# Performance work log

Hardware: AMD Instinct MI355X
Metric: run time of the kernel (lower is better)

## Reference

```python
import jax, jax.numpy as jnp
import numpy as np

# --- module constants (from init_kwargs) ---
R_HRS = 1000000.0   # high-resistance state (ohm)
R_LRS = 1000.0      # low-resistance state (ohm)
PARASITIC_R = 2.0   # wire resistance per crossbar segment (ohm)
BITS = 4            # conductance quantization bits
BATCH, IN_F, OUT_F = 8192, 1024, 1024


def weight_mapping(W, R_hrs, R_lrs):
    # linearly map weights into the [G_hrs, G_lrs] conductance window
    G_hrs, G_lrs = 1.0 / R_hrs, 1.0 / R_lrs
    Wmin, Wmax = W.min(), W.max()
    return (W - Wmin) / (Wmax - Wmin) * (G_lrs - G_hrs) + G_hrs


def quantization(G, R_lrs, R_hrs, bits):
    # snap conductances to 2**bits uniform levels in [G_hrs, G_lrs]
    G_hrs, G_lrs = 1.0 / R_hrs, 1.0 / R_lrs
    step = (G_lrs - G_hrs) / (2 ** bits - 1)
    return jnp.round((G - G_hrs) / step) * step + G_hrs


def ideal_model(G, x, parasitic_r):
    # ideal crossbar: I = V @ G  (no IR drop)
    return x @ G


def jeong_model(G, x, parasitic_r):
    # Jeong-style analytical IR-drop model: each cell (i, j) sees an extra
    # series wire resistance r*((j+1) segments along its word line +
    # (rows - i) segments along its bit line).
    rows, cols = G.shape  # [in, out]
    r_series = parasitic_r * (
        (jnp.arange(cols, dtype=G.dtype) + 1.0)[None, :]
        + (rows - jnp.arange(rows, dtype=G.dtype))[:, None]
    )  # [in, out]
    G_eff = 1.0 / (1.0 / G + r_series)
    return x @ G_eff  # [batch, out]


def output_unmapping(Wt, currents, x, R_hrs, R_lrs):
    # invert the affine conductance mapping: G = a*W + b  =>  x@W = (I - b*sum(x))/a
    G_hrs, G_lrs = 1.0 / R_hrs, 1.0 / R_lrs
    Wmin, Wmax = Wt.min(), Wt.max()
    a = (G_lrs - G_hrs) / (Wmax - Wmin)
    b = G_hrs - a * Wmin
    return (currents - b * x.sum(axis=1, keepdims=True)) / a


def setup_inputs() -> dict:
    key = jax.random.key(0)
    k1, k2, k3 = jax.random.split(key, 3)
    x = jax.random.uniform(k1, (BATCH, IN_F), dtype=jnp.float32)          # read voltages in [0,1)
    weight = jax.random.normal(k2, (OUT_F, IN_F), dtype=jnp.float32) * 0.1
    bias = jax.random.normal(k3, (OUT_F,), dtype=jnp.float32) * 0.01
    return {"x": x, "weight": weight, "bias": bias}


def reference(x, weight, bias):
    Wt = weight.T  # [in, out], matches self.weight.T in the torch module
    conductances = quantization(weight_mapping(Wt, R_HRS, R_LRS), R_LRS, R_HRS, BITS)
    currents = jeong_model(conductances, x, PARASITIC_R)          # non-ideal simulation
    ideal_currents = ideal_model(conductances, x, PARASITIC_R)    # bias-correction pass
    correction = currents.mean(axis=1) / ideal_currents.mean(axis=1)  # [batch]
    output = output_unmapping(Wt, currents, x, R_HRS, R_LRS)      # [batch, out]
    return output + bias[None, :] * correction[:, None]
```

## Files before the change

### kernel.cpp

```cpp
#include <hip/hip_runtime.h>
#include <hip/hip_bf16.h>
#include <cstdint>

#define BATCH 8192
#define IN_F  1024
#define OUT_F 1024
#define G_HRS 1e-6f
#define G_LRS 1e-3f
#define PAR_R 2.0f
#define LEVELS 15.0f

#define WS_PMIN  0
#define WS_PMAX  1024
#define WS_VEFF  4096
#define WS_VID   8192
#define WS_CORR  16384
#define WS_BT    65536
#define WS_ABF   (65536 + 2097152)
#define WS_NEED_FULL  ((size_t)WS_ABF + (size_t)BATCH * IN_F * 2)

__device__ __forceinline__ unsigned short f2bf(float f) {
    union { float f; unsigned int i; } v; v.f = f;
    unsigned int u = v.i;
    unsigned int r = (u + 0x7FFFu + ((u >> 16) & 1u)) >> 16;
    return (unsigned short)r;
}
__device__ __forceinline__ float quant_g(float wv, float wmin, float inv_range) {
    float t = (wv - wmin) * inv_range;
    float step = (G_LRS - G_HRS) / LEVELS;
    return rintf(t * LEVELS) * step + G_HRS;
}

__global__ void kprep(const float* __restrict__ w, float* __restrict__ pmin, float* __restrict__ pmax,
                      float* __restrict__ veff, float* __restrict__ vid) {
    int tid = blockIdx.x * blockDim.x + threadIdx.x;
    float lo = 1e30f, hi = -1e30f;
    const float4* w4 = (const float4*)w;
    const int n4 = (IN_F * OUT_F) / 4;
    for (int i = tid; i < n4; i += 256 * 256) {
        float4 q = w4[i];
        lo = fminf(lo, fminf(fminf(q.x, q.y), fminf(q.z, q.w)));
        hi = fmaxf(hi, fmaxf(fmaxf(q.x, q.y), fmaxf(q.z, q.w)));
    }
#pragma unroll
    for (int m = 1; m < 64; m <<= 1) {
        lo = fminf(lo, __shfl_xor(lo, m, 64));
        hi = fmaxf(hi, __shfl_xor(hi, m, 64));
    }
    __shared__ float slo[4], shi[4];
    int wv = threadIdx.x >> 6, ln = threadIdx.x & 63;
    if (ln == 0) { slo[wv] = lo; shi[wv] = hi; }
    __syncthreads();
    if (threadIdx.x == 0) {
        pmin[blockIdx.x] = fminf(fminf(slo[0], slo[1]), fminf(slo[2], slo[3]));
        pmax[blockIdx.x] = fmaxf(fmaxf(shi[0], shi[1]), fmaxf(shi[2], shi[3]));
    }
    if (blockIdx.x == 0) {
        float4 z = make_float4(0.f, 0.f, 0.f, 0.f);
        ((float4*)veff)[threadIdx.x] = z;
        ((float4*)vid)[threadIdx.x]  = z;
    }
}

__global__ void kbuildvec(const float* __restrict__ w, const float* __restrict__ pmin,
                          const float* __restrict__ pmax, unsigned short* __restrict__ bt,
                          float* __restrict__ veff, float* __restrict__ vid) {
    float lo = pmin[threadIdx.x], hi = pmax[threadIdx.x];
#pragma unroll
    for (int m = 1; m < 64; m <<= 1) {
        lo = fminf(lo, __shfl_xor(lo, m, 64));
        hi = fmaxf(hi, __shfl_xor(hi, m, 64));
    }
    __shared__ float slo[4], shi[4];
    int wv = threadIdx.x >> 6, ln = threadIdx.x & 63;
    if (ln == 0) { slo[wv] = lo; shi[wv] = hi; }
    __syncthreads();
    float wmin = fminf(fminf(slo[0], slo[1]), fminf(slo[2], slo[3]));
    float wmax = fmaxf(fmaxf(shi[0], shi[1]), fmaxf(shi[2], shi[3]));

    float inv_range = 1.0f / (wmax - wmin);
    float acoef = (G_LRS - G_HRS) * inv_range;
    float bcoef = G_HRS - acoef * wmin;
    float inva = 1.0f / acoef;

    int k0 = threadIdx.x * 4;
    float se[4] = {0.f, 0.f, 0.f, 0.f}, si[4] = {0.f, 0.f, 0.f, 0.f};
#pragma unroll
    for (int rr = 0; rr < 16; rr++) {
        int n = blockIdx.x * 16 + rr;
        float4 q = *(const float4*)&w[(size_t)n * IN_F + k0];
        float wvv[4] = { q.x, q.y, q.z, q.w };
        unsigned short o[4];
#pragma unroll
        for (int j = 0; j < 4; j++) {
            int k = k0 + j;
            float g = quant_g(wvv[j], wmin, inv_range);
            float r = PAR_R * ((float)(n + 1) + (float)(IN_F - k));
            float ge = 1.0f / (1.0f / g + r);
            o[j] = f2bf((ge - bcoef) * inva);
            se[j] += ge;
            si[j] += g;
        }
        uint2 ov;
        ov.x = (unsigned int)o[0] | ((unsigned int)o[1] << 16);
        ov.y = (unsigned int)o[2] | ((unsigned int)o[3] << 16);
        *(uint2*)&bt[(size_t)n * IN_F + k0] = ov;
    }
#pragma unroll
    for (int j = 0; j < 4; j++) {
        atomicAdd(&veff[k0 + j], se[j]);
        atomicAdd(&vid[k0 + j], si[j]);
    }
}

__global__ void kcorr(const float* __restrict__ x, const float* __restrict__ veff,
                      const float* __restrict__ vid, float* __restrict__ corr,
                      unsigned short* __restrict__ abf) {
    int row = blockIdx.x * 4 + (threadIdx.x >> 6);
    int lane = threadIdx.x & 63;
    const float* xr = x + (size_t)row * IN_F;
    float se = 0.f, si = 0.f;
#pragma unroll
    for (int p = 0; p < 4; p++) {
        int off = p * 256 + lane * 4;
        float4 q  = *(const float4*)(xr + off);
        float4 ve = *(const float4*)(veff + off);
        float4 vi = *(const float4*)(vid  + off);
        se += q.x * ve.x + q.y * ve.y + q.z * ve.z + q.w * ve.w;
        si += q.x * vi.x + q.y * vi.y + q.z * vi.z + q.w * vi.w;
        if (abf) {
            uint2 ov;
            ov.x = (unsigned int)f2bf(q.x) | ((unsigned int)f2bf(q.y) << 16);
            ov.y = (unsigned int)f2bf(q.z) | ((unsigned int)f2bf(q.w) << 16);
            *(uint2*)&abf[(size_t)row * IN_F + off] = ov;
        }
    }
#pragma unroll
    for (int m = 1; m < 64; m <<= 1) {
        se += __shfl_xor(se, m, 64);
        si += __shfl_xor(si, m, 64);
    }
    if (lane == 0) corr[row] = se / si;
}

typedef __attribute__((ext_vector_type(8))) short bf16x8;
typedef __attribute__((ext_vector_type(4))) float f32x4;

#define GLD_LDS16(g, l) \
    __builtin_amdgcn_global_load_lds((const __attribute__((address_space(1))) void*)(g), \
                                     (__attribute__((address_space(3))) void*)(l), 16, 0, 0)

#define SCHED0   __builtin_amdgcn_sched_barrier(0)
#define LGKM(n)  do { asm volatile("s_waitcnt lgkmcnt(" #n ")" ::: "memory"); SCHED0; } while (0)
#define VMCNT(n) asm volatile("s_waitcnt vmcnt(" #n ")" ::: "memory")
#define SBAR     asm volatile("s_barrier" ::: "memory")

#define MFMA_ROW4(MT, A, B0, B1, B2, B3) \
    acc[MT][0] = __builtin_amdgcn_mfma_f32_16x16x32_bf16(A, B0, acc[MT][0], 0, 0, 0); \
    acc[MT][1] = __builtin_amdgcn_mfma_f32_16x16x32_bf16(A, B1, acc[MT][1], 0, 0, 0); \
    acc[MT][2] = __builtin_amdgcn_mfma_f32_16x16x32_bf16(A, B2, acc[MT][2], 0, 0, 0); \
    acc[MT][3] = __builtin_amdgcn_mfma_f32_16x16x32_bf16(A, B3, acc[MT][3], 0, 0, 0);

__global__ __launch_bounds__(256) void kgemm2(
    const unsigned short* __restrict__ Abf,
    const unsigned short* __restrict__ Bt,
    const float* __restrict__ bias,
    const float* __restrict__ corr,
    float* __restrict__ out)
{
    __shared__ unsigned short As[2 * 128 * 64];
    __shared__ unsigned short Bs[2 * 128 * 64];
    const int tid = threadIdx.x;
    const int f = blockIdx.x;
    const int bm = ((f & 7) * 8 + ((f >> 3) & 7)) * 128;
    const int bn = (f >> 6) * 128;
    const int wave = tid >> 6, lane = tid & 63;
    const int wmL = (wave >> 1) * 64;
    const int wnL = (wave & 1) * 64;
    const int fr = lane & 15;
    const int quad = lane >> 4;

    const int sw   = (fr & 7) * 16;
    const int aRd0 = (wmL + fr) * 128 + ((quad * 16) ^ sw);
    const int aRd1 = (wmL + fr) * 128 + (((64 + quad * 16)) ^ sw);
    const int bRd0 = (wnL + fr) * 128 + ((quad * 16) ^ sw);
    const int bRd1 = (wnL + fr) * 128 + (((64 + quad * 16)) ^ sw);

    const int arow  = tid >> 3;
    const int acolb = ((tid & 7) * 16) ^ ((arow & 7) * 16);
    const unsigned short* gA = Abf + (size_t)(bm + arow) * IN_F + (acolb >> 1);
    const unsigned short* gB = Bt  + (size_t)(bn + arow) * IN_F + (acolb >> 1);

    f32x4 acc[4][4] = {};

    {
        unsigned short* lA = As + tid * 8;
        unsigned short* lB = Bs + tid * 8;
        GLD_LDS16(gB,              lB);
        GLD_LDS16(gB + 32 * IN_F,  lB + 2048);
        GLD_LDS16(gB + 64 * IN_F,  lB + 4096);
        GLD_LDS16(gB + 96 * IN_F,  lB + 6144);
        GLD_LDS16(gA,              lA);
        GLD_LDS16(gA + 32 * IN_F,  lA + 2048);
        GLD_LDS16(gA + 64 * IN_F,  lA + 4096);
        GLD_LDS16(gA + 96 * IN_F,  lA + 6144);
        VMCNT(0);
        SBAR;
    }

#pragma unroll 1
    for (int t = 0; t < 15; ++t) {
        const int rb = (t & 1) << 13;
        const int wb = rb ^ 8192;
        const int kbn = t * 64 + 64;
        const char* Ar = (const char*)(As + rb);
        const char* Br = (const char*)(Bs + rb);
        unsigned short* Aw = As + wb + tid * 8;
        unsigned short* Bw = Bs + wb + tid * 8;
        bf16x8 b0, b1, b2, b3, a0, a1;
        bf16x8 c0, c1, c2, c3, p0, p1;
        bf16x8 q0, q1;

        b0 = *(const bf16x8*)(Br + bRd0);
        b1 = *(const bf16x8*)(Br + bRd0 + 2048);
        b2 = *(const bf16x8*)(Br + bRd0 + 4096);
        b3 = *(const bf16x8*)(Br + bRd0 + 6144);
        a0 = *(const bf16x8*)(Ar + aRd0);
        a1 = *(const bf16x8*)(Ar + aRd0 + 2048);
        SCHED0;
        c0 = *(const bf16x8*)(Br + bRd1);
        c1 = *(const bf16x8*)(Br + bRd1 + 2048);
        c2 = *(const bf16x8*)(Br + bRd1 + 4096);
        c3 = *(const bf16x8*)(Br + bRd1 + 6144);
        p0 = *(const bf16x8*)(Ar + aRd1);
        p1 = *(const bf16x8*)(Ar + aRd1 + 2048);
        GLD_LDS16(gB + kbn,             Bw);
        GLD_LDS16(gB + 32 * IN_F + kbn, Bw + 2048);
        LGKM(6);
        __builtin_amdgcn_s_setprio(1);
        MFMA_ROW4(0, a0, b0, b1, b2, b3)
        MFMA_ROW4(1, a1, b0, b1, b2, b3)
        __builtin_amdgcn_s_setprio(0);
        SCHED0;
        VMCNT(2);
        SBAR;

        a0 = *(const bf16x8*)(Ar + aRd0 + 4096);
        a1 = *(const bf16x8*)(Ar + aRd0 + 6144);
        SCHED0;
        q0 = *(const bf16x8*)(Ar + aRd1 + 4096);
        q1 = *(const bf16x8*)(Ar + aRd1 + 6144);
        GLD_LDS16(gB + 64 * IN_F + kbn, Bw + 4096);
        GLD_LDS16(gB + 96 * IN_F + kbn, Bw + 6144);
        LGKM(2);
        __builtin_amdgcn_s_setprio(1);
        MFMA_ROW4(2, a0, b0, b1, b2, b3)
        MFMA_ROW4(3, a1, b0, b1, b2, b3)
        __builtin_amdgcn_s_setprio(0);
        SCHED0;

        GLD_LDS16(gA + kbn,             Aw);
        GLD_LDS16(gA + 64 * IN_F + kbn, Aw + 4096);
        LGKM(2);
        __builtin_amdgcn_s_setprio(1);
        MFMA_ROW4(0, p0, c0, c1, c2, c3)
        MFMA_ROW4(1, p1, c0, c1, c2, c3)
        __builtin_amdgcn_s_setprio(0);
        SCHED0;

        GLD_LDS16(gA + 32 * IN_F + kbn, Aw + 2048);
        GLD_LDS16(gA + 96 * IN_F + kbn, Aw + 6144);
        LGKM(0);
        __builtin_amdgcn_s_setprio(1);
        MFMA_ROW4(2, q0, c0, c1, c2, c3)
        MFMA_ROW4(3, q1, c0, c1, c2, c3)
        __builtin_amdgcn_s_setprio(0);
        SCHED0;
        VMCNT(2);
        SBAR;
    }

    {
        const char* Ar = (const char*)(As + 8192);
        const char* Br = (const char*)(Bs + 8192);
        bf16x8 b0, b1, b2, b3, a0, a1;

        b0 = *(const bf16x8*)(Br + bRd0);
        b1 = *(const bf16x8*)(Br + bRd0 + 2048);
        b2 = *(const bf16x8*)(Br + bRd0 + 4096);
        b3 = *(const bf16x8*)(Br + bRd0 + 6144);
        a0 = *(const bf16x8*)(Ar + aRd0);
        a1 = *(const bf16x8*)(Ar + aRd0 + 2048);
        LGKM(0);
        __builtin_amdgcn_s_setprio(1);
        MFMA_ROW4(0, a0, b0, b1, b2, b3)
        MFMA_ROW4(1, a1, b0, b1, b2, b3)
        __builtin_amdgcn_s_setprio(0);
        SCHED0;
        VMCNT(0);
        SBAR;

        a0 = *(const bf16x8*)(Ar + aRd0 + 4096);
        a1 = *(const bf16x8*)(Ar + aRd0 + 6144);
        LGKM(0);
        __builtin_amdgcn_s_setprio(1);
        MFMA_ROW4(2, a0, b0, b1, b2, b3)
        MFMA_ROW4(3, a1, b0, b1, b2, b3)
        __builtin_amdgcn_s_setprio(0);
        SCHED0;

        b0 = *(const bf16x8*)(Br + bRd1);
        b1 = *(const bf16x8*)(Br + bRd1 + 2048);
        b2 = *(const bf16x8*)(Br + bRd1 + 4096);
        b3 = *(const bf16x8*)(Br + bRd1 + 6144);
        a0 = *(const bf16x8*)(Ar + aRd1);
        a1 = *(const bf16x8*)(Ar + aRd1 + 2048);
        LGKM(0);
        __builtin_amdgcn_s_setprio(1);
        MFMA_ROW4(0, a0, b0, b1, b2, b3)
        MFMA_ROW4(1, a1, b0, b1, b2, b3)
        __builtin_amdgcn_s_setprio(0);
        SCHED0;

        a0 = *(const bf16x8*)(Ar + aRd1 + 4096);
        a1 = *(const bf16x8*)(Ar + aRd1 + 6144);
        LGKM(0);
        __builtin_amdgcn_s_setprio(1);
        MFMA_ROW4(2, a0, b0, b1, b2, b3)
        MFMA_ROW4(3, a1, b0, b1, b2, b3)
        __builtin_amdgcn_s_setprio(0);
        SCHED0;
    }

#pragma unroll
    for (int nt = 0; nt < 4; nt++) {
        int gc = bn + wnL + nt * 16 + fr;
        float bv = bias[gc];
#pragma unroll
        for (int mt = 0; mt < 4; mt++) {
#pragma unroll
            for (int r = 0; r < 4; r++) {
                int gr = bm + wmL + mt * 16 + quad * 4 + r;
                out[(size_t)gr * OUT_F + gc] = acc[mt][nt][r] + bv * corr[gr];
            }
        }
    }
}

__global__ __launch_bounds__(256) void kgemm_conva(
    const float* __restrict__ Af32,
    const unsigned short* __restrict__ Bt,
    const float* __restrict__ bias,
    const float* __restrict__ corr,
    float* __restrict__ out)
{
    __shared__ unsigned short As0[128 * 32];
    __shared__ unsigned short As1[128 * 32];
    __shared__ unsigned short Bs0[128 * 32];
    __shared__ unsigned short Bs1[128 * 32];
    const int tid = threadIdx.x;
    const int f = blockIdx.x;
    const int bm = ((f & 7) * 8 + ((f >> 3) & 7)) * 128;
    const int bn = (f >> 6) * 128;
    const int wave = tid >> 6, lane = tid & 63;
    const int wmL = (wave >> 1) * 64;
    const int wnL = (wave & 1) * 64;
    const int fr = lane & 15;
    const int fk = (lane >> 4) * 8;
    const int quad = lane >> 4;

    f32x4 acc[4][4] = {};

    const int c0 = tid, c1 = tid + 256;
    const unsigned short* gB0 = Bt + (size_t)(bn + (c0 >> 2)) * IN_F + ((c0 & 3) << 3);
    const unsigned short* gB1 = Bt + (size_t)(bn + (c1 >> 2)) * IN_F + ((c1 & 3) << 3);
    const float* fA0 = Af32 + (size_t)(bm + (c0 >> 2)) * IN_F + ((c0 & 3) << 3);
    const float* fA1 = Af32 + (size_t)(bm + (c1 >> 2)) * IN_F + ((c1 & 3) << 3);

    for (int kb = 0; kb < IN_F; kb += 64) {
        float4 p[8];
        p[0] = *(const float4*)(fA0 + kb);      p[1] = *(const float4*)(fA0 + kb + 4);
        p[2] = *(const float4*)(fA1 + kb);      p[3] = *(const float4*)(fA1 + kb + 4);
        p[4] = *(const float4*)(fA0 + kb + 32); p[5] = *(const float4*)(fA0 + kb + 36);
        p[6] = *(const float4*)(fA1 + kb + 32); p[7] = *(const float4*)(fA1 + kb + 36);
        uint4 u[4];
#pragma unroll
        for (int j = 0; j < 4; j++) {
            u[j] = make_uint4(
                (unsigned int)f2bf(p[2*j].x) | ((unsigned int)f2bf(p[2*j].y) << 16),
                (unsigned int)f2bf(p[2*j].z) | ((unsigned int)f2bf(p[2*j].w) << 16),
                (unsigned int)f2bf(p[2*j+1].x) | ((unsigned int)f2bf(p[2*j+1].y) << 16),
                (unsigned int)f2bf(p[2*j+1].z) | ((unsigned int)f2bf(p[2*j+1].w) << 16));
        }
        __syncthreads();
        *(uint4*)&As0[c0 * 8] = u[0];
        *(uint4*)&As0[c1 * 8] = u[1];
        *(uint4*)&As1[c0 * 8] = u[2];
        *(uint4*)&As1[c1 * 8] = u[3];
        GLD_LDS16(gB0 + kb, &Bs0[c0 * 8]);
        GLD_LDS16(gB1 + kb, &Bs0[c1 * 8]);
        GLD_LDS16(gB0 + kb + 32, &Bs1[c0 * 8]);
        GLD_LDS16(gB1 + kb + 32, &Bs1[c1 * 8]);
        __syncthreads();

        bf16x8 af[4], bfv[4];
#pragma unroll
        for (int mt = 0; mt < 4; mt++)
            af[mt] = *(const bf16x8*)&As0[(wmL + mt * 16 + fr) * 32 + fk];
#pragma unroll
        for (int nt = 0; nt < 4; nt++)
            bfv[nt] = *(const bf16x8*)&Bs0[(wnL + nt * 16 + fr) * 32 + fk];
#pragma unroll
        for (int mt = 0; mt < 4; mt++)
#pragma unroll
            for (int nt = 0; nt < 4; nt++)
                acc[mt][nt] = __builtin_amdgcn_mfma_f32_16x16x32_bf16(af[mt], bfv[nt], acc[mt][nt], 0, 0, 0);
#pragma unroll
        for (int mt = 0; mt < 4; mt++)
            af[mt] = *(const bf16x8*)&As1[(wmL + mt * 16 + fr) * 32 + fk];
#pragma unroll
        for (int nt = 0; nt < 4; nt++)
            bfv[nt] = *(const bf16x8*)&Bs1[(wnL + nt * 16 + fr) * 32 + fk];
#pragma unroll
        for (int mt = 0; mt < 4; mt++)
#pragma unroll
            for (int nt = 0; nt < 4; nt++)
                acc[mt][nt] = __builtin_amdgcn_mfma_f32_16x16x32_bf16(af[mt], bfv[nt], acc[mt][nt], 0, 0, 0);
    }

#pragma unroll
    for (int nt = 0; nt < 4; nt++) {
        int gc = bn + wnL + nt * 16 + fr;
        float bv = bias[gc];
#pragma unroll
        for (int mt = 0; mt < 4; mt++) {
#pragma unroll
            for (int r = 0; r < 4; r++) {
                int gr = bm + wmL + mt * 16 + quad * 4 + r;
                out[(size_t)gr * OUT_F + gc] = acc[mt][nt][r] + bv * corr[gr];
            }
        }
    }
}

extern "C" void kernel_launch(void* const* d_in, const int* in_sizes, int n_in,
                              void* d_out, int out_size, void* d_ws, size_t ws_size,
                              hipStream_t stream) {
    const float* x    = (const float*)d_in[0];
    const float* w    = (const float*)d_in[1];
    const float* bias = (const float*)d_in[2];
    float* out = (float*)d_out;

    char* ws = (char*)d_ws;
    float* pmin        = (float*)(ws + WS_PMIN);
    float* pmax        = (float*)(ws + WS_PMAX);
    float* veff        = (float*)(ws + WS_VEFF);
    float* vid         = (float*)(ws + WS_VID);
    float* corr        = (float*)(ws + WS_CORR);
    unsigned short* bt = (unsigned short*)(ws + WS_BT);
    unsigned short* abf = (unsigned short*)(ws + WS_ABF);

    bool full = ws_size >= WS_NEED_FULL;

    kprep<<<256, 256, 0, stream>>>(w, pmin, pmax, veff, vid);
    kbuildvec<<<OUT_F / 16, 256, 0, stream>>>(w, pmin, pmax, bt, veff, vid);
    kcorr<<<BATCH / 4, 256, 0, stream>>>(x, veff, vid, corr, full ? abf : nullptr);
    if (full)
        kgemm2<<<512, 256, 0, stream>>>(abf, bt, bias, corr, out);
    else
        kgemm_conva<<<512, 256, 0, stream>>>(x, bt, bias, corr, out);
}
```

Before: 126.1 us.

## Fuse prep kernels into one cooperative kernel and reschedule GEMM global loads

Merges the three front-end kernels (min/max reduction, conductance build, correction/bf16 conversion) into one cooperative kernel with grid-wide syncs, removing two launch gaps and hoisting the veff/vid loads out of the row loop. It also moves the B and A global-to-LDS prefetches earlier in the GEMM main loop and adjusts the vmcnt wait to overlap more loads with MFMA. Cooperative launch needs all 512 blocks co-resident, and grid.sync adds its own cost. Issuing loads earlier may add pressure on LDS and memory queues.

```diff
diff --git a/kernel.cpp b/kernel.cpp
--- a/kernel.cpp
+++ b/kernel.cpp
@@ -1,6 +1,9 @@
 #include <hip/hip_runtime.h>
 #include <hip/hip_bf16.h>
+#include <hip/hip_cooperative_groups.h>
 #include <cstdint>
+
+namespace cg = cooperative_groups;
 
 #define BATCH 8192
 #define IN_F  1024
@@ -11,7 +14,7 @@
 #define LEVELS 15.0f
 
 #define WS_PMIN  0
-#define WS_PMAX  1024
+#define WS_PMAX  2048
 #define WS_VEFF  4096
 #define WS_VID   8192
 #define WS_CORR  16384
@@ -31,116 +34,129 @@
     return rintf(t * LEVELS) * step + G_HRS;
 }
 
-__global__ void kprep(const float* __restrict__ w, float* __restrict__ pmin, float* __restrict__ pmax,
-                      float* __restrict__ veff, float* __restrict__ vid) {
-    int tid = blockIdx.x * blockDim.x + threadIdx.x;
-    float lo = 1e30f, hi = -1e30f;
-    const float4* w4 = (const float4*)w;
-    const int n4 = (IN_F * OUT_F) / 4;
-    for (int i = tid; i < n4; i += 256 * 256) {
-        float4 q = w4[i];
-        lo = fminf(lo, fminf(fminf(q.x, q.y), fminf(q.z, q.w)));
-        hi = fmaxf(hi, fmaxf(fmaxf(q.x, q.y), fmaxf(q.z, q.w)));
-    }
-#pragma unroll
-    for (int m = 1; m < 64; m <<= 1) {
-        lo = fminf(lo, __shfl_xor(lo, m, 64));
-        hi = fmaxf(hi, __shfl_xor(hi, m, 64));
-    }
+__global__ void kfront(const float* __restrict__ w, const float* __restrict__ x,
+                       float* __restrict__ pmin, float* __restrict__ pmax,
+                       float* __restrict__ veff, float* __restrict__ vid,
+                       unsigned short* __restrict__ bt, float* __restrict__ corr,
+                       unsigned short* __restrict__ abf) {
+    cg::grid_group grid = cg::this_grid();
+    const int tid = threadIdx.x;
+    const int bid = blockIdx.x;
+    const int wv = tid >> 6, ln = tid & 63;
     __shared__ float slo[4], shi[4];
-    int wv = threadIdx.x >> 6, ln = threadIdx.x & 63;
-    if (ln == 0) { slo[wv] = lo; shi[wv] = hi; }
-    __syncthreads();
-    if (threadIdx.x == 0) {
-        pmin[blockIdx.x] = fminf(fminf(slo[0], slo[1]), fminf(slo[2], slo[3]));
-        pmax[blockIdx.x] = fmaxf(fmaxf(shi[0], shi[1]), fmaxf(shi[2], shi[3]));
-    }
-    if (blockIdx.x == 0) {
-        float4 z = make_float4(0.f, 0.f, 0.f, 0.f);
-        ((float4*)veff)[threadIdx.x] = z;
-        ((float4*)vid)[threadIdx.x]  = z;
-    }
-}
-
-__global__ void kbuildvec(const float* __restrict__ w, const float* __restrict__ pmin,
-                          const float* __restrict__ pmax, unsigned short* __restrict__ bt,
-                          float* __restrict__ veff, float* __restrict__ vid) {
-    float lo = pmin[threadIdx.x], hi = pmax[threadIdx.x];
-#pragma unroll
-    for (int m = 1; m < 64; m <<= 1) {
-        lo = fminf(lo, __shfl_xor(lo, m, 64));
-        hi = fmaxf(hi, __shfl_xor(hi, m, 64));
-    }
-    __shared__ float slo[4], shi[4];
-    int wv = threadIdx.x >> 6, ln = threadIdx.x & 63;
-    if (ln == 0) { slo[wv] = lo; shi[wv] = hi; }
-    __syncthreads();
-    float wmin = fminf(fminf(slo[0], slo[1]), fminf(slo[2], slo[3]));
-    float wmax = fmaxf(fmaxf(shi[0], shi[1]), fmaxf(shi[2], shi[3]));
-
-    float inv_range = 1.0f / (wmax - wmin);
-    float acoef = (G_LRS - G_HRS) * inv_range;
-    float bcoef = G_HRS - acoef * wmin;
-    float inva = 1.0f / acoef;
-
-    int k0 = threadIdx.x * 4;
-    float se[4] = {0.f, 0.f, 0.f, 0.f}, si[4] = {0.f, 0.f, 0.f, 0.f};
-#pragma unroll
-    for (int rr = 0; rr < 16; rr++) {
-        int n = blockIdx.x * 16 + rr;
-        float4 q = *(const float4*)&w[(size_t)n * IN_F + k0];
-        float wvv[4] = { q.x, q.y, q.z, q.w };
-        unsigned short o[4];
+
+    {
+        float lo = 1e30f, hi = -1e30f;
+        const float4* w4 = (const float4*)w;
+        const int n4 = (IN_F * OUT_F) / 4;
+        for (int i = bid * 256 + tid; i < n4; i += 512 * 256) {
+            float4 q = w4[i];
+            lo = fminf(lo, fminf(fminf(q.x, q.y), fminf(q.z, q.w)));
+            hi = fmaxf(hi, fmaxf(fmaxf(q.x, q.y), fmaxf(q.z, q.w)));
+        }
+#pragma unroll
+        for (int m = 1; m < 64; m <<= 1) {
+            lo = fminf(lo, __shfl_xor(lo, m, 64));
+            hi = fmaxf(hi, __shfl_xor(hi, m, 64));
+        }
+        if (ln == 0) { slo[wv] = lo; shi[wv] = hi; }
+        __syncthreads();
+        if (tid == 0) {
+            pmin[bid] = fminf(fminf(slo[0], slo[1]), fminf(slo[2], slo[3]));
+            pmax[bid] = fmaxf(fmaxf(shi[0], shi[1]), fmaxf(shi[2], shi[3]));
+        }
+        if (bid == 0) {
+            float4 z = make_float4(0.f, 0.f, 0.f, 0.f);
+            ((float4*)veff)[tid] = z;
+            ((float4*)vid)[tid]  = z;
+        }
+    }
+    grid.sync();
+
+    if (bid < 64) {
+        float lo = fminf(pmin[tid], pmin[tid + 256]);
+        float hi = fmaxf(pmax[tid], pmax[tid + 256]);
+#pragma unroll
+        for (int m = 1; m < 64; m <<= 1) {
+            lo = fminf(lo, __shfl_xor(lo, m, 64));
+            hi = fmaxf(hi, __shfl_xor(hi, m, 64));
+        }
+        if (ln == 0) { slo[wv] = lo; shi[wv] = hi; }
+        __syncthreads();
+        float wmin = fminf(fminf(slo[0], slo[1]), fminf(slo[2], slo[3]));
+        float wmax = fmaxf(fmaxf(shi[0], shi[1]), fmaxf(shi[2], shi[3]));
+
+        float inv_range = 1.0f / (wmax - wmin);
+        float acoef = (G_LRS - G_HRS) * inv_range;
+        float bcoef = G_HRS - acoef * wmin;
+        float inva = 1.0f / acoef;
+
+        int k0 = tid * 4;
+        float se[4] = {0.f, 0.f, 0.f, 0.f}, si[4] = {0.f, 0.f, 0.f, 0.f};
+#pragma unroll
+        for (int rr = 0; rr < 16; rr++) {
+            int n = bid * 16 + rr;
+            float4 q = *(const float4*)&w[(size_t)n * IN_F + k0];
+            float wvv[4] = { q.x, q.y, q.z, q.w };
+            unsigned short o[4];
+#pragma unroll
+            for (int j = 0; j < 4; j++) {
+                int k = k0 + j;
+                float g = quant_g(wvv[j], wmin, inv_range);
+                float r = PAR_R * ((float)(n + 1) + (float)(IN_F - k));
+                float ge = 1.0f / (1.0f / g + r);
+                o[j] = f2bf((ge - bcoef) * inva);
+                se[j] += ge;
+                si[j] += g;
+            }
+            uint2 ov;
+            ov.x = (unsigned int)o[0] | ((unsigned int)o[1] << 16);
+            ov.y = (unsigned int)o[2] | ((unsigned int)o[3] << 16);
+            *(uint2*)&bt[(size_t)n * IN_F + k0] = ov;
+        }
 #pragma unroll
         for (int j = 0; j < 4; j++) {
-            int k = k0 + j;
-            float g = quant_g(wvv[j], wmin, inv_range);
-            float r = PAR_R * ((float)(n + 1) + (float)(IN_F - k));
-            float ge = 1.0f / (1.0f / g + r);
-            o[j] = f2bf((ge - bcoef) * inva);
-            se[j] += ge;
-            si[j] += g;
-        }
-        uint2 ov;
-        ov.x = (unsigned int)o[0] | ((unsigned int)o[1] << 16);
-        ov.y = (unsigned int)o[2] | ((unsigned int)o[3] << 16);
-        *(uint2*)&bt[(size_t)n * IN_F + k0] = ov;
-    }
-#pragma unroll
-    for (int j = 0; j < 4; j++) {
-        atomicAdd(&veff[k0 + j], se[j]);
-        atomicAdd(&vid[k0 + j], si[j]);
-    }
-}
-
-__global__ void kcorr(const float* __restrict__ x, const float* __restrict__ veff,
-                      const float* __restrict__ vid, float* __restrict__ corr,
-                      unsigned short* __restrict__ abf) {
-    int row = blockIdx.x * 4 + (threadIdx.x >> 6);
-    int lane = threadIdx.x & 63;
-    const float* xr = x + (size_t)row * IN_F;
-    float se = 0.f, si = 0.f;
-#pragma unroll
-    for (int p = 0; p < 4; p++) {
-        int off = p * 256 + lane * 4;
-        float4 q  = *(const float4*)(xr + off);
-        float4 ve = *(const float4*)(veff + off);
-        float4 vi = *(const float4*)(vid  + off);
-        se += q.x * ve.x + q.y * ve.y + q.z * ve.z + q.w * ve.w;
-        si += q.x * vi.x + q.y * vi.y + q.z * vi.z + q.w * vi.w;
-        if (abf) {
-            uint2 ov;
-            ov.x = (unsigned int)f2bf(q.x) | ((unsigned int)f2bf(q.y) << 16);
-            ov.y = (unsigned int)f2bf(q.z) | ((unsigned int)f2bf(q.w) << 16);
-            *(uint2*)&abf[(size_t)row * IN_F + off] = ov;
-        }
-    }
-#pragma unroll
-    for (int m = 1; m < 64; m <<= 1) {
-        se += __shfl_xor(se, m, 64);
-        si += __shfl_xor(si, m, 64);
-    }
-    if (lane == 0) corr[row] = se / si;
+            atomicAdd(&veff[k0 + j], se[j]);
+            atomicAdd(&vid[k0 + j], si[j]);
+        }
+    }
+    grid.sync();
+
+    {
+        const int lane = ln;
+        float4 ve[4], vi[4];
+#pragma unroll
+        for (int p = 0; p < 4; p++) {
+            int off = p * 256 + lane * 4;
+            ve[p] = *(const float4*)(veff + off);
+            vi[p] = *(const float4*)(vid  + off);
+        }
+#pragma unroll 2
+        for (int it = 0; it < 4; it++) {
+            int row = bid * 16 + it * 4 + wv;
+            const float* xr = x + (size_t)row * IN_F;
+            float se = 0.f, si = 0.f;
+#pragma unroll
+            for (int p = 0; p < 4; p++) {
+                int off = p * 256 + lane * 4;
+                float4 q = *(const float4*)(xr + off);
+                se += q.x * ve[p].x + q.y * ve[p].y + q.z * ve[p].z + q.w * ve[p].w;
+                si += q.x * vi[p].x + q.y * vi[p].y + q.z * vi[p].z + q.w * vi[p].w;
+                if (abf) {
+                    uint2 ov;
+                    ov.x = (unsigned int)f2bf(q.x) | ((unsigned int)f2bf(q.y) << 16);
+                    ov.y = (unsigned int)f2bf(q.z) | ((unsigned int)f2bf(q.w) << 16);
+                    *(uint2*)&abf[(size_t)row * IN_F + off] = ov;
+                }
+            }
+#pragma unroll
+            for (int m = 1; m < 64; m <<= 1) {
+                se += __shfl_xor(se, m, 64);
+                si += __shfl_xor(si, m, 64);
+            }
+            if (lane == 0) corr[row] = se / si;
+        }
+    }
 }
 
 typedef __attribute__((ext_vector_type(8))) short bf16x8;
@@ -236,13 +252,15 @@
         p1 = *(const bf16x8*)(Ar + aRd1 + 2048);
         GLD_LDS16(gB + kbn,             Bw);
         GLD_LDS16(gB + 32 * IN_F + kbn, Bw + 2048);
+        GLD_LDS16(gB + 64 * IN_F + kbn, Bw + 4096);
+        GLD_LDS16(gB + 96 * IN_F + kbn, Bw + 6144);
         LGKM(6);
         __builtin_amdgcn_s_setprio(1);
         MFMA_ROW4(0, a0, b0, b1, b2, b3)
         MFMA_ROW4(1, a1, b0, b1, b2, b3)
         __builtin_amdgcn_s_setprio(0);
         SCHED0;
-        VMCNT(2);
+        VMCNT(4);
         SBAR;
 
         a0 = *(const bf16x8*)(Ar + aRd0 + 4096);
@@ -250,8 +268,11 @@
         SCHED0;
         q0 = *(const bf16x8*)(Ar + aRd1 + 4096);
         q1 = *(const bf16x8*)(Ar + aRd1 + 6144);
-        GLD_LDS16(gB + 64 * IN_F + kbn, Bw + 4096);
-        GLD_LDS16(gB + 96 * IN_F + kbn, Bw + 6144);
+        GLD_LDS16(gA + kbn,             Aw);
+        GLD_LDS16(gA + 64 * IN_F + kbn, Aw + 4096);
+        SCHED0;
+        GLD_LDS16(gA + 32 * IN_F + kbn, Aw + 2048);
+        GLD_LDS16(gA + 96 * IN_F + kbn, Aw + 6144);
         LGKM(2);
         __builtin_amdgcn_s_setprio(1);
         MFMA_ROW4(2, a0, b0, b1, b2, b3)
@@ -259,8 +280,6 @@
         __builtin_amdgcn_s_setprio(0);
         SCHED0;
 
-        GLD_LDS16(gA + kbn,             Aw);
-        GLD_LDS16(gA + 64 * IN_F + kbn, Aw + 4096);
         LGKM(2);
         __builtin_amdgcn_s_setprio(1);
         MFMA_ROW4(0, p0, c0, c1, c2, c3)
@@ -268,8 +287,6 @@
         __builtin_amdgcn_s_setprio(0);
         SCHED0;
 
-        GLD_LDS16(gA + 32 * IN_F + kbn, Aw + 2048);
-        GLD_LDS16(gA + 96 * IN_F + kbn, Aw + 6144);
         LGKM(0);
         __builtin_amdgcn_s_setprio(1);
         MFMA_ROW4(2, q0, c0, c1, c2, c3)
@@ -461,10 +478,14 @@
     unsigned short* abf = (unsigned short*)(ws + WS_ABF);
 
     bool full = ws_size >= WS_NEED_FULL;
-
-    kprep<<<256, 256, 0, stream>>>(w, pmin, pmax, veff, vid);
-    kbuildvec<<<OUT_F / 16, 256, 0, stream>>>(w, pmin, pmax, bt, veff, vid);
-    kcorr<<<BATCH / 4, 256, 0, stream>>>(x, veff, vid, corr, full ? abf : nullptr);
+    unsigned short* abf_arg = full ? abf : nullptr;
+
+    void* args[] = { (void*)&w, (void*)&x, (void*)&pmin, (void*)&pmax,
+                     (void*)&veff, (void*)&vid, (void*)&bt, (void*)&corr,
+                     (void*)&abf_arg };
+    hipLaunchCooperativeKernel((const void*)kfront, dim3(512), dim3(256),
+                               args, 0, stream);
+
     if (full)
         kgemm2<<<512, 256, 0, stream>>>(abf, bt, bias, corr, out);
     else
```

Measured after the change: 228.9 us. +81.5%, slower.
